# Optimization experiments

Hardware: AMD Instinct MI355X
Metric: run time of the kernel (lower is better)

## Reference

```python
import jax, jax.numpy as jnp
import numpy as np

B, H, N, T, E, D = 8, 8, 64, 256, 512, 64  # batch, heads, series, window, embed, feature
TAU = 1.0
DH = E // H  # per-head dim = 64


def setup_inputs() -> dict:
    key = jax.random.key(0)
    ks = jax.random.split(key, 7)
    f32 = jnp.float32
    return {
        "q": jax.random.normal(ks[0], (B, N, E), f32),
        "k": jax.random.normal(ks[1], (B, N, E), f32),
        "v": jax.random.normal(ks[2], (B, H, N, T, D), f32),
        # nn.Linear weights use torch (out, in) convention, bias=False
        "Wq": jax.random.normal(ks[3], (E, E), f32) * (E ** -0.5),
        "Wk": jax.random.normal(ks[4], (E, E), f32) * (E ** -0.5),
        # causal-convolution temporal mixing kernel per head/series
        "Wconv": jax.random.normal(ks[5], (H, N, T, T), f32) * (T ** -0.5),
        # concat projection: (out=D, in=H*D)
        "Wcat": jax.random.normal(ks[6], (D, H * D), f32) * ((H * D) ** -0.5),
    }


def reference(q, k, v, Wq, Wk, Wconv, Wcat):
    # Q/K projections, split into heads: (B,N,E) -> (B,H,N,DH)
    Q = (q @ Wq.T).reshape(B, N, H, DH).transpose(0, 2, 1, 3)
    K = (k @ Wk.T).reshape(B, N, H, DH).transpose(0, 2, 1, 3)

    # Causal convolution V projection: lower-triangular masked temporal mixing
    causal = jnp.tril(jnp.ones((T, T), v.dtype))
    V = jnp.einsum('hnts,bhnsd->bhntd', Wconv * causal, v)  # (B,H,N,T,D)

    # tau-scaled multi-head attention over the series axis
    scores = jnp.einsum('bhid,bhjd->bhij', Q, K) / (TAU * np.sqrt(DH).astype(np.float32))
    attn = jax.nn.softmax(scores, axis=-1)  # (B,H,N,N); dropout=0 (eval)
    out = jnp.einsum('bhij,bhjtd->bhitd', attn, V)  # (B,H,N,T,D)

    # reshape/permute chain == (B,H,N,T,D) -> (B,N,T,H*D)
    out = out.transpose(0, 2, 3, 1, 4).reshape(B, N, T, H * D)
    return out @ Wcat.T  # (B,N,T,D)
```

## Files before the change

kernel.cpp:

```cpp
#include <hip/hip_runtime.h>
#include <hip/hip_bf16.h>


typedef unsigned short u16;
typedef unsigned int u32;
typedef __attribute__((ext_vector_type(8))) short short8;
typedef __attribute__((ext_vector_type(4))) float f32x4;

static __device__ __forceinline__ u16 f2bf(float f) {
    u32 x; __builtin_memcpy(&x, &f, 4);
    u32 r = (x + 0x7fffu + ((x >> 16) & 1u)) >> 16;
    return (u16)r;
}
static __device__ __forceinline__ short8 pack8(float4 a, float4 b) {
    short8 r;
    r[0] = (short)f2bf(a.x); r[1] = (short)f2bf(a.y);
    r[2] = (short)f2bf(a.z); r[3] = (short)f2bf(a.w);
    r[4] = (short)f2bf(b.x); r[5] = (short)f2bf(b.y);
    r[6] = (short)f2bf(b.z); r[7] = (short)f2bf(b.w);
    return r;
}
static __device__ __forceinline__ short8 mk_bfrag(f32x4 a, f32x4 b) {
    u32 w0 = (__float_as_uint(a[0]) >> 16) | (__float_as_uint(a[1]) & 0xffff0000u);
    u32 w1 = (__float_as_uint(a[2]) >> 16) | (__float_as_uint(a[3]) & 0xffff0000u);
    u32 w2 = (__float_as_uint(b[0]) >> 16) | (__float_as_uint(b[1]) & 0xffff0000u);
    u32 w3 = (__float_as_uint(b[2]) >> 16) | (__float_as_uint(b[3]) & 0xffff0000u);
    uint4 u = make_uint4(w0, w1, w2, w3);
    short8 r; __builtin_memcpy(&r, &u, 16); return r;
}
static __device__ __forceinline__ short8 mk_bfrag_rnd(f32x4 a, f32x4 b) {
    short8 r;
    r[0] = (short)f2bf(a[0]); r[1] = (short)f2bf(a[1]);
    r[2] = (short)f2bf(a[2]); r[3] = (short)f2bf(a[3]);
    r[4] = (short)f2bf(b[0]); r[5] = (short)f2bf(b[1]);
    r[6] = (short)f2bf(b[2]); r[7] = (short)f2bf(b[3]);
    return r;
}
static __device__ __forceinline__ uint2 pk4(f32x4 d) {
    return make_uint2((__float_as_uint(d[0]) >> 16) | (__float_as_uint(d[1]) & 0xffff0000u),
                      (__float_as_uint(d[2]) >> 16) | (__float_as_uint(d[3]) & 0xffff0000u));
}

__global__ __launch_bounds__(256) void proj_qk(
        const float* __restrict__ q, const float* __restrict__ k,
        const float* __restrict__ Wq, const float* __restrict__ Wk,
        float* __restrict__ Qh, float* __restrict__ Kh) {
    const int et = blockIdx.x, rt = blockIdx.y, z = blockIdx.z;
    const float* X = z ? k : q;
    const float* W = z ? Wk : Wq;
    float* Out = z ? Kh : Qh;
    __shared__ float Xs[32][65];
    __shared__ float Ws[32][65];
    const int tid = threadIdx.x;
    const int tx = tid & 15, ty = tid >> 4;
    const int r0 = rt * 64, e0 = et * 64;
    float acc[4][4] = {};
    for (int k0 = 0; k0 < 512; k0 += 32) {
        __syncthreads();
        #pragma unroll
        for (int rep = 0; rep < 8; ++rep) {
            int lin = rep * 256 + tid;
            int kk = lin & 31, m = lin >> 5;
            Xs[kk][m] = X[(size_t)(r0 + m) * 512 + k0 + kk];
            Ws[kk][m] = W[(size_t)(e0 + m) * 512 + k0 + kk];
        }
        __syncthreads();
        #pragma unroll 8
        for (int kk = 0; kk < 32; ++kk) {
            float a0 = Xs[kk][4 * ty + 0], a1 = Xs[kk][4 * ty + 1];
            float a2 = Xs[kk][4 * ty + 2], a3 = Xs[kk][4 * ty + 3];
            float b0 = Ws[kk][4 * tx + 0], b1 = Ws[kk][4 * tx + 1];
            float b2 = Ws[kk][4 * tx + 2], b3 = Ws[kk][4 * tx + 3];
            acc[0][0] += a0 * b0; acc[0][1] += a0 * b1; acc[0][2] += a0 * b2; acc[0][3] += a0 * b3;
            acc[1][0] += a1 * b0; acc[1][1] += a1 * b1; acc[1][2] += a1 * b2; acc[1][3] += a1 * b3;
            acc[2][0] += a2 * b0; acc[2][1] += a2 * b1; acc[2][2] += a2 * b2; acc[2][3] += a2 * b3;
            acc[3][0] += a3 * b0; acc[3][1] += a3 * b1; acc[3][2] += a3 * b2; acc[3][3] += a3 * b3;
        }
    }
    #pragma unroll
    for (int i = 0; i < 4; ++i) {
        #pragma unroll
        for (int j = 0; j < 4; ++j) {
            int r = r0 + 4 * ty + i;
            int e = e0 + 4 * tx + j;
            int b = r >> 6, n = r & 63, h = e >> 6, dh = e & 63;
            Out[(((size_t)(b * 8 + h) * 64 + n) * 64) + dh] = acc[i][j];
        }
    }
}

__global__ __launch_bounds__(256) void attn_softmax(
        const float* __restrict__ Qh, const float* __restrict__ Kh,
        u16* __restrict__ Aperm) {
    const int bh = blockIdx.x;
    const int b = bh >> 3, h = bh & 7;
    const int tid = threadIdx.x;
    __shared__ float Qt[64][64];
    __shared__ float KT[64][65];
    const size_t base = (size_t)bh * 4096;
    #pragma unroll
    for (int rep = 0; rep < 16; ++rep) {
        int lin = rep * 256 + tid;
        int r = lin >> 6, c = lin & 63;
        Qt[r][c] = Qh[base + lin];
        KT[c][r] = Kh[base + lin];
    }
    __syncthreads();
    const int w = tid >> 6, lane = tid & 63;
    const int w31 = lane & 31;
    const int slot = (w31 < 16) ? ((w31 >> 2) * 8 + (w31 & 3))
                                : (((w31 - 16) >> 2) * 8 + 4 + (w31 & 3));
    const int p = h * 64 + (lane & 32) + slot;
    for (int rr = 0; rr < 16; ++rr) {
        int i = w + 4 * rr;
        float s = 0.f;
        #pragma unroll
        for (int dd = 0; dd < 64; ++dd) s += Qt[i][dd] * KT[dd][lane];
        s *= 0.125f;
        float m = s;
        #pragma unroll
        for (int off = 32; off; off >>= 1) m = fmaxf(m, __shfl_xor(m, off));
        float e = __expf(s - m);
        float sum = e;
        #pragma unroll
        for (int off = 32; off; off >>= 1) sum += __shfl_xor(sum, off);
        Aperm[((size_t)(b * 64 + i) << 9) + p] = f2bf(e / sum);
    }
}

template<int TI, int OFF>
__device__ __forceinline__ void load_tile(short8 wc[18], const float* __restrict__ wcb,
                                          int lo, int hi) {
    const int t = TI * 16 + lo;
    #pragma unroll
    for (int kk = 0; kk <= TI / 2; ++kk) {
        const float* p = wcb + (size_t)t * 256 + kk * 32 + hi * 8;
        float4 x = ((const float4*)p)[0], y = ((const float4*)p)[1];
        float wf[8] = {x.x, x.y, x.z, x.w, y.x, y.y, y.z, y.w};
        if (kk == TI / 2) {
            int sb = kk * 32 + hi * 8;
            #pragma unroll
            for (int e = 0; e < 8; ++e)
                if (sb + e > t) wf[e] = 0.f;
        }
        short8 af;
        #pragma unroll
        for (int e = 0; e < 8; ++e) af[e] = (short)f2bf(wf[e]);
        wc[OFF + kk] = af;
    }
}

template<int W>
__device__ __forceinline__ void load_wconv_w(short8 wc[18], const float* __restrict__ wcb,
                                             int lo, int hi) {
    load_tile<2 * W,      0        >(wc, wcb, lo, hi);
    load_tile<2 * W + 1,  W + 1    >(wc, wcb, lo, hi);
    load_tile<14 - 2 * W, 2 * W + 2>(wc, wcb, lo, hi);
    load_tile<15 - 2 * W, 10 + W   >(wc, wcb, lo, hi);
}

template<int M, int OA, int OB, int TB>
__device__ __forceinline__ void pair_conv_store(const short8 wc[18],
        const u16* __restrict__ vptB, u16* __restrict__ vout,
        int lo, int hi, short8 J1, short8 J2) {
    f32x4 aA[4] = {}, aB[4] = {};
    #pragma unroll
    for (int kk = 0; kk <= M; ++kk) {
        short8 bfr[4];
        #pragma unroll
        for (int di = 0; di < 4; ++di) {
            int d = di * 16 + lo;
            int sc = kk * 4 + hi;
            bfr[di] = *(const short8*)&vptB[d * 256 + ((sc ^ (d & 7)) << 3)];
        }
        #pragma unroll
        for (int di = 0; di < 4; ++di) {
            aA[di] = __builtin_amdgcn_mfma_f32_16x16x32_bf16(wc[OA + kk], bfr[di], aA[di], 0, 0, 0);
            aB[di] = __builtin_amdgcn_mfma_f32_16x16x32_bf16(wc[OB + kk], bfr[di], aB[di], 0, 0, 0);
        }
    }
    const f32x4 z = {};
    #pragma unroll
    for (int di = 0; di < 4; ++di) {
        short8 Xc = mk_bfrag_rnd(aA[di], aB[di]);
        f32x4 D1 = __builtin_amdgcn_mfma_f32_16x16x32_bf16(Xc, J1, z, 0, 0, 0);
        f32x4 D2 = __builtin_amdgcn_mfma_f32_16x16x32_bf16(Xc, J2, z, 0, 0, 0);
        *(uint2*)&vout[(size_t)(TB + lo) * 64 + di * 16 + hi * 4] = pk4(D1);
        *(uint2*)&vout[(size_t)(TB + 16 + lo) * 64 + di * 16 + hi * 4] = pk4(D2);
    }
}

template<int W>
__device__ __forceinline__ void phaseB_w(const short8 wc[18], const u16* __restrict__ vptB,
        u16* __restrict__ vout, int lo, int hi, short8 J1, short8 J2) {
    pair_conv_store<W,     0,         W + 1,  32 * W       >(wc, vptB, vout, lo, hi, J1, J2);
    pair_conv_store<7 - W, 2 * W + 2, 10 + W, (14 - 2 * W) * 16>(wc, vptB, vout, lo, hi, J1, J2);
}

__global__ __launch_bounds__(256, 2) void conv_mfma(
        const float* __restrict__ v, const float* __restrict__ Wconv,
        const float* __restrict__ Wcat, u16* __restrict__ Vp,
        int b0, int bs, int nsplit) {
    const int bid = blockIdx.x;
    const int split = (nsplit > 1) ? ((bid >> 3) & 1) : 0;
    const int hj = (nsplit > 1) ? (((bid >> 4) << 3) | (bid & 7)) : bid;
    const int h = hj >> 6, j = hj & 63;
    const int tid = threadIdx.x;
    const int w = tid >> 6, l = tid & 63;
    const int lo = l & 15, hi = l >> 4;
    const int bstart = b0 + split * bs;
    const int blbase = split * bs;

    __shared__ u16 vptB[2][64 * 256];

    short8 J1, J2;
    #pragma unroll
    for (int e = 0; e < 8; ++e) {
        int pie = (e < 4) ? (hi * 4 + e) : (16 + hi * 4 + (e - 4));
        J1[e] = (pie == lo) ? (short)0x3F80 : (short)0;
        J2[e] = (pie == lo + 16) ? (short)0x3F80 : (short)0;
    }

    short8 wc[18];
    const float* wcb = Wconv + (size_t)hj * 65536;
    if (w == 0)      load_wconv_w<0>(wc, wcb, lo, hi);
    else if (w == 1) load_wconv_w<1>(wc, wcb, lo, hi);
    else if (w == 2) load_wconv_w<2>(wc, wcb, lo, hi);
    else             load_wconv_w<3>(wc, wcb, lo, hi);

    short8 wcat[2][4];
    #pragma unroll
    for (int kk = 0; kk < 2; ++kk)
        #pragma unroll
        for (int di = 0; di < 4; ++di) {
            const float* p = Wcat + (size_t)(di * 16 + lo) * 512 + h * 64 + kk * 32 + hi * 8;
            wcat[kk][di] = pack8(((const float4*)p)[0], ((const float4*)p)[1]);
        }

    for (int i = 0; i < bs; ++i) {
        const int b = bstart + i;
        u16* buf = vptB[i & 1];
        const size_t vb = ((size_t)(b * 8 + h) * 64 + j) * 16384;
        #pragma unroll
        for (int si = 0; si < 4; ++si) {
            const float* p = v + vb + (size_t)(w * 64 + si * 16 + lo) * 64;
            f32x4 a4[4] = {};
            #pragma unroll
            for (int kk = 0; kk < 2; ++kk) {
                const float4* q = (const float4*)(p + kk * 32 + hi * 8);
                short8 af = pack8(q[0], q[1]);
                #pragma unroll
                for (int di = 0; di < 4; ++di)
                    a4[di] = __builtin_amdgcn_mfma_f32_16x16x32_bf16(af, wcat[kk][di], a4[di], 0, 0, 0);
            }
            int s0 = w * 64 + si * 16 + hi * 4;
            #pragma unroll
            for (int di = 0; di < 4; ++di) {
                int d = di * 16 + lo;
                u32 lo32 = (u32)f2bf(a4[di][0]) | ((u32)f2bf(a4[di][1]) << 16);
                u32 hi32 = (u32)f2bf(a4[di][2]) | ((u32)f2bf(a4[di][3]) << 16);
                *(uint2*)&buf[d * 256 + (((s0 >> 3) ^ (d & 7)) << 3) + (s0 & 7)] =
                    make_uint2(lo32, hi32);
            }
        }
        __syncthreads();
        u16* vout = Vp + ((size_t)(blbase + i) * 512 + hj) * 16384;
        if (w == 0)      phaseB_w<0>(wc, buf, vout, lo, hi, J1, J2);
        else if (w == 1) phaseB_w<1>(wc, buf, vout, lo, hi, J1, J2);
        else if (w == 2) phaseB_w<2>(wc, buf, vout, lo, hi, J1, J2);
        else             phaseB_w<3>(wc, buf, vout, lo, hi, J1, J2);
    }
}

__global__ __launch_bounds__(256) void final_mfma(
        const u16* __restrict__ Aperm, const u16* __restrict__ Vp,
        float* __restrict__ out, int bbase) {
    const int nblk = blockIdx.x;
    const int bl = blockIdx.y, b = bbase + bl;
    const int tid = threadIdx.x;
    const int w = tid >> 6, l = tid & 63;
    const int lo = l & 15, hi = l >> 4;
    const int nb = nblk * 128 + w * 32;

    short8 I1, I2;
    #pragma unroll
    for (int e = 0; e < 8; ++e) {
        I1[e] = (hi * 8 + e == lo) ? (short)0x3F80 : (short)0;
        I2[e] = (hi * 8 + e == lo + 16) ? (short)0x3F80 : (short)0;
    }

    const u16* ab = Aperm + ((size_t)b << 15);
    const u16* vb = Vp + (size_t)bl * 512 * 16384;

    f32x4 acc[4][2] = {};
    const f32x4 z = {};

    #define LDAF(af, k0) { \
        _Pragma("unroll") \
        for (int mi = 0; mi < 4; ++mi) \
            af[mi] = *(const short8*)&ab[(size_t)(mi * 16 + lo) * 512 + (k0) + hi * 8]; }
    #define LDX(X1, X2, k0) { \
        X1 = *(const short8*)&vb[(size_t)((k0) + lo) * 16384 + nb + hi * 8]; \
        X2 = *(const short8*)&vb[(size_t)((k0) + 16 + lo) * 16384 + nb + hi * 8]; }
    #define COMPUTE(af, X1, X2) { \
        f32x4 t1a = __builtin_amdgcn_mfma_f32_16x16x32_bf16(X1, I1, z, 0, 0, 0); \
        f32x4 t1b = __builtin_amdgcn_mfma_f32_16x16x32_bf16(X1, I2, z, 0, 0, 0); \
        f32x4 t2a = __builtin_amdgcn_mfma_f32_16x16x32_bf16(X2, I1, z, 0, 0, 0); \
        f32x4 t2b = __builtin_amdgcn_mfma_f32_16x16x32_bf16(X2, I2, z, 0, 0, 0); \
        short8 B0 = mk_bfrag(t1a, t2a); \
        short8 B1 = mk_bfrag(t1b, t2b); \
        _Pragma("unroll") \
        for (int mi = 0; mi < 4; ++mi) { \
            acc[mi][0] = __builtin_amdgcn_mfma_f32_16x16x32_bf16(af[mi], B0, acc[mi][0], 0, 0, 0); \
            acc[mi][1] = __builtin_amdgcn_mfma_f32_16x16x32_bf16(af[mi], B1, acc[mi][1], 0, 0, 0); \
        } }

    short8 afA[4], afB[4], X1A, X2A, X1B, X2B;
    LDAF(afA, 0); LDX(X1A, X2A, 0);
    #pragma unroll
    for (int ks = 0; ks < 16; ks += 2) {
        const int k1 = (ks + 1) * 32;
        const int k2 = ((ks + 2) & 15) * 32;
        LDAF(afB, k1); LDX(X1B, X2B, k1);
        COMPUTE(afA, X1A, X2A);
        LDAF(afA, k2); LDX(X1A, X2A, k2);
        COMPUTE(afB, X1B, X2B);
    }
    #undef LDAF
    #undef LDX
    #undef COMPUTE

    float* ob = out + ((size_t)b << 20);
    #pragma unroll
    for (int mi = 0; mi < 4; ++mi) {
        #pragma unroll
        for (int nt = 0; nt < 2; ++nt) {
            int td = nb + nt * 16 + lo;
            #pragma unroll
            for (int r = 0; r < 4; ++r) {
                int i = mi * 16 + hi * 4 + r;
                ob[(size_t)i * 16384 + td] = acc[mi][nt][r];
            }
        }
    }
}

extern "C" void kernel_launch(void* const* d_in, const int* in_sizes, int n_in,
                              void* d_out, int out_size, void* d_ws, size_t ws_size,
                              hipStream_t stream) {
    const float* q     = (const float*)d_in[0];
    const float* k     = (const float*)d_in[1];
    const float* v     = (const float*)d_in[2];
    const float* Wq    = (const float*)d_in[3];
    const float* Wk    = (const float*)d_in[4];
    const float* Wconv = (const float*)d_in[5];
    const float* Wcat  = (const float*)d_in[6];
    float* out = (float*)d_out;

    u16* Aperm = (u16*)d_ws;
    float* Qh = (float*)(Aperm + 262144);
    float* Kh = Qh + 262144;
    u16* Vp = (u16*)(Kh + 262144);
    const size_t fixed = 262144 * 2 + (size_t)2 * 262144 * 4;

    int bc = 8;
    while (bc > 1 && fixed + (size_t)bc * 512 * 16384 * 2 > ws_size) bc >>= 1;

    proj_qk<<<dim3(8, 8, 2), 256, 0, stream>>>(q, k, Wq, Wk, Qh, Kh);
    attn_softmax<<<64, 256, 0, stream>>>(Qh, Kh, Aperm);
    for (int b0 = 0; b0 < 8; b0 += bc) {
        int nsplit = (bc + 3) / 4;
        int bs = bc / nsplit;
        conv_mfma<<<dim3(nsplit * 512), 256, 0, stream>>>(v, Wconv, Wcat, Vp, b0, bs, nsplit);
        final_mfma<<<dim3(128, bc), 256, 0, stream>>>(Aperm, Vp, out, b0);
    }
}
```

Baseline: 226.2 us.

## Split conv work across eight waves per block and stage Wcat in LDS

The causal-conv kernel now runs 512 threads (8 waves) per (head,series) block instead of 4 waves, with each wave owning one paired time tile (W and 15-W), so Wconv registers per wave drop from 18 to 9 fragments. The batch split across two blocks is removed, so each block loops over all batches in its chunk with a single LDS buffer guarded by extra barriers. Wcat is packed once into swizzled LDS and reread per batch instead of being held in registers. The aim is more waves resident per CU and lower register pressure, at the cost of fewer blocks (512) and an added barrier per iteration that drops the double-buffer overlap.

Measured after the change: 219.6 us, median of 2. 1.03x faster.

```diff
diff --git a/kernel.cpp b/kernel.cpp
--- a/kernel.cpp
+++ b/kernel.cpp
@@ -129,7 +129,7 @@
 }
 
 template<int TI, int OFF>
-__device__ __forceinline__ void load_tile(short8 wc[18], const float* __restrict__ wcb,
+__device__ __forceinline__ void load_tile(short8* wc, const float* __restrict__ wcb,
                                           int lo, int hi) {
     const int t = TI * 16 + lo;
     #pragma unroll
@@ -151,21 +151,19 @@
 }
 
 template<int W>
-__device__ __forceinline__ void load_wconv_w(short8 wc[18], const float* __restrict__ wcb,
+__device__ __forceinline__ void load_wconv_w(short8 wc[9], const float* __restrict__ wcb,
                                              int lo, int hi) {
-    load_tile<2 * W,      0        >(wc, wcb, lo, hi);
-    load_tile<2 * W + 1,  W + 1    >(wc, wcb, lo, hi);
-    load_tile<14 - 2 * W, 2 * W + 2>(wc, wcb, lo, hi);
-    load_tile<15 - 2 * W, 10 + W   >(wc, wcb, lo, hi);
-}
-
-template<int M, int OA, int OB, int TB>
-__device__ __forceinline__ void pair_conv_store(const short8 wc[18],
-        const u16* __restrict__ vptB, u16* __restrict__ vout,
-        int lo, int hi, short8 J1, short8 J2) {
+    load_tile<W,      0        >(wc, wcb, lo, hi);
+    load_tile<15 - W, W / 2 + 1>(wc, wcb, lo, hi);
+}
+
+template<int W>
+__device__ __forceinline__ void phaseB_w(const short8 wc[9], const u16* __restrict__ vptB,
+        u16* __restrict__ vout, int lo, int hi, short8 J1) {
+    constexpr int KA = W / 2, KB = (15 - W) / 2, OB = KA + 1;
     f32x4 aA[4] = {}, aB[4] = {};
     #pragma unroll
-    for (int kk = 0; kk <= M; ++kk) {
+    for (int kk = 0; kk <= KB; ++kk) {
         short8 bfr[4];
         #pragma unroll
         for (int di = 0; di < 4; ++di) {
@@ -175,100 +173,111 @@
         }
         #pragma unroll
         for (int di = 0; di < 4; ++di) {
-            aA[di] = __builtin_amdgcn_mfma_f32_16x16x32_bf16(wc[OA + kk], bfr[di], aA[di], 0, 0, 0);
             aB[di] = __builtin_amdgcn_mfma_f32_16x16x32_bf16(wc[OB + kk], bfr[di], aB[di], 0, 0, 0);
+            if (kk <= KA)
+                aA[di] = __builtin_amdgcn_mfma_f32_16x16x32_bf16(wc[kk], bfr[di], aA[di], 0, 0, 0);
         }
     }
     const f32x4 z = {};
     #pragma unroll
     for (int di = 0; di < 4; ++di) {
-        short8 Xc = mk_bfrag_rnd(aA[di], aB[di]);
-        f32x4 D1 = __builtin_amdgcn_mfma_f32_16x16x32_bf16(Xc, J1, z, 0, 0, 0);
-        f32x4 D2 = __builtin_amdgcn_mfma_f32_16x16x32_bf16(Xc, J2, z, 0, 0, 0);
-        *(uint2*)&vout[(size_t)(TB + lo) * 64 + di * 16 + hi * 4] = pk4(D1);
-        *(uint2*)&vout[(size_t)(TB + 16 + lo) * 64 + di * 16 + hi * 4] = pk4(D2);
-    }
-}
-
-template<int W>
-__device__ __forceinline__ void phaseB_w(const short8 wc[18], const u16* __restrict__ vptB,
-        u16* __restrict__ vout, int lo, int hi, short8 J1, short8 J2) {
-    pair_conv_store<W,     0,         W + 1,  32 * W       >(wc, vptB, vout, lo, hi, J1, J2);
-    pair_conv_store<7 - W, 2 * W + 2, 10 + W, (14 - 2 * W) * 16>(wc, vptB, vout, lo, hi, J1, J2);
-}
-
-__global__ __launch_bounds__(256, 2) void conv_mfma(
+        short8 XcA = mk_bfrag_rnd(aA[di], aA[di]);
+        short8 XcB = mk_bfrag_rnd(aB[di], aB[di]);
+        f32x4 DA = __builtin_amdgcn_mfma_f32_16x16x32_bf16(XcA, J1, z, 0, 0, 0);
+        f32x4 DB = __builtin_amdgcn_mfma_f32_16x16x32_bf16(XcB, J1, z, 0, 0, 0);
+        *(uint2*)&vout[(size_t)(W * 16 + lo) * 64 + di * 16 + hi * 4] = pk4(DA);
+        *(uint2*)&vout[(size_t)((15 - W) * 16 + lo) * 64 + di * 16 + hi * 4] = pk4(DB);
+    }
+}
+
+__global__ __launch_bounds__(512, 4) void conv_mfma(
         const float* __restrict__ v, const float* __restrict__ Wconv,
         const float* __restrict__ Wcat, u16* __restrict__ Vp,
-        int b0, int bs, int nsplit) {
-    const int bid = blockIdx.x;
-    const int split = (nsplit > 1) ? ((bid >> 3) & 1) : 0;
-    const int hj = (nsplit > 1) ? (((bid >> 4) << 3) | (bid & 7)) : bid;
-    const int h = hj >> 6, j = hj & 63;
+        int b0, int bs) {
+    const int hj = blockIdx.x, h = hj >> 6, j = hj & 63;
     const int tid = threadIdx.x;
     const int w = tid >> 6, l = tid & 63;
     const int lo = l & 15, hi = l >> 4;
-    const int bstart = b0 + split * bs;
-    const int blbase = split * bs;
-
-    __shared__ u16 vptB[2][64 * 256];
-
-    short8 J1, J2;
+
+    __shared__ u16 vptB[64 * 256];
+    __shared__ u16 wcatL[64 * 64];
+
+    short8 J1;
     #pragma unroll
     for (int e = 0; e < 8; ++e) {
         int pie = (e < 4) ? (hi * 4 + e) : (16 + hi * 4 + (e - 4));
         J1[e] = (pie == lo) ? (short)0x3F80 : (short)0;
-        J2[e] = (pie == lo + 16) ? (short)0x3F80 : (short)0;
-    }
-
-    short8 wc[18];
+    }
+
+    short8 wc[9];
     const float* wcb = Wconv + (size_t)hj * 65536;
     if (w == 0)      load_wconv_w<0>(wc, wcb, lo, hi);
     else if (w == 1) load_wconv_w<1>(wc, wcb, lo, hi);
     else if (w == 2) load_wconv_w<2>(wc, wcb, lo, hi);
-    else             load_wconv_w<3>(wc, wcb, lo, hi);
-
-    short8 wcat[2][4];
-    #pragma unroll
-    for (int kk = 0; kk < 2; ++kk)
-        #pragma unroll
-        for (int di = 0; di < 4; ++di) {
-            const float* p = Wcat + (size_t)(di * 16 + lo) * 512 + h * 64 + kk * 32 + hi * 8;
-            wcat[kk][di] = pack8(((const float4*)p)[0], ((const float4*)p)[1]);
-        }
+    else if (w == 3) load_wconv_w<3>(wc, wcb, lo, hi);
+    else if (w == 4) load_wconv_w<4>(wc, wcb, lo, hi);
+    else if (w == 5) load_wconv_w<5>(wc, wcb, lo, hi);
+    else if (w == 6) load_wconv_w<6>(wc, wcb, lo, hi);
+    else             load_wconv_w<7>(wc, wcb, lo, hi);
+
+    {
+        int lin = tid * 8;
+        int d = lin >> 6, dd0 = lin & 63;
+        const float* p = Wcat + (size_t)d * 512 + h * 64 + dd0;
+        short8 wv = pack8(((const float4*)p)[0], ((const float4*)p)[1]);
+        *(short8*)&wcatL[d * 64 + (((dd0 >> 3) ^ (d & 7)) << 3)] = wv;
+    }
+    asm volatile("s_waitcnt lgkmcnt(0)" ::: "memory");
+    __builtin_amdgcn_s_barrier();
 
     for (int i = 0; i < bs; ++i) {
-        const int b = bstart + i;
-        u16* buf = vptB[i & 1];
+        const int b = b0 + i;
+        short8 wcat[2][4];
+        #pragma unroll
+        for (int kk = 0; kk < 2; ++kk)
+            #pragma unroll
+            for (int di = 0; di < 4; ++di) {
+                int d = di * 16 + lo;
+                int c8 = kk * 4 + hi;
+                wcat[kk][di] = *(const short8*)&wcatL[d * 64 + ((c8 ^ (d & 7)) << 3)];
+            }
         const size_t vb = ((size_t)(b * 8 + h) * 64 + j) * 16384;
         #pragma unroll
-        for (int si = 0; si < 4; ++si) {
-            const float* p = v + vb + (size_t)(w * 64 + si * 16 + lo) * 64;
+        for (int si = 0; si < 2; ++si) {
+            const float* p = v + vb + (size_t)(w * 32 + si * 16 + lo) * 64;
+            const float4* q0 = (const float4*)(p + hi * 8);
+            const float4* q1 = (const float4*)(p + 32 + hi * 8);
+            short8 af0 = pack8(q0[0], q0[1]);
+            short8 af1 = pack8(q1[0], q1[1]);
             f32x4 a4[4] = {};
             #pragma unroll
-            for (int kk = 0; kk < 2; ++kk) {
-                const float4* q = (const float4*)(p + kk * 32 + hi * 8);
-                short8 af = pack8(q[0], q[1]);
-                #pragma unroll
-                for (int di = 0; di < 4; ++di)
-                    a4[di] = __builtin_amdgcn_mfma_f32_16x16x32_bf16(af, wcat[kk][di], a4[di], 0, 0, 0);
+            for (int di = 0; di < 4; ++di) {
+                a4[di] = __builtin_amdgcn_mfma_f32_16x16x32_bf16(af0, wcat[0][di], a4[di], 0, 0, 0);
+                a4[di] = __builtin_amdgcn_mfma_f32_16x16x32_bf16(af1, wcat[1][di], a4[di], 0, 0, 0);
             }
-            int s0 = w * 64 + si * 16 + hi * 4;
+            int s0 = w * 32 + si * 16 + hi * 4;
             #pragma unroll
             for (int di = 0; di < 4; ++di) {
                 int d = di * 16 + lo;
                 u32 lo32 = (u32)f2bf(a4[di][0]) | ((u32)f2bf(a4[di][1]) << 16);
                 u32 hi32 = (u32)f2bf(a4[di][2]) | ((u32)f2bf(a4[di][3]) << 16);
-                *(uint2*)&buf[d * 256 + (((s0 >> 3) ^ (d & 7)) << 3) + (s0 & 7)] =
+                *(uint2*)&vptB[d * 256 + (((s0 >> 3) ^ (d & 7)) << 3) + (s0 & 7)] =
                     make_uint2(lo32, hi32);
             }
         }
-        __syncthreads();
-        u16* vout = Vp + ((size_t)(blbase + i) * 512 + hj) * 16384;
-        if (w == 0)      phaseB_w<0>(wc, buf, vout, lo, hi, J1, J2);
-        else if (w == 1) phaseB_w<1>(wc, buf, vout, lo, hi, J1, J2);
-        else if (w == 2) phaseB_w<2>(wc, buf, vout, lo, hi, J1, J2);
-        else             phaseB_w<3>(wc, buf, vout, lo, hi, J1, J2);
+        asm volatile("s_waitcnt lgkmcnt(0)" ::: "memory");
+        __builtin_amdgcn_s_barrier();
+        u16* vout = Vp + ((size_t)i * 512 + hj) * 16384;
+        if (w == 0)      phaseB_w<0>(wc, vptB, vout, lo, hi, J1);
+        else if (w == 1) phaseB_w<1>(wc, vptB, vout, lo, hi, J1);
+        else if (w == 2) phaseB_w<2>(wc, vptB, vout, lo, hi, J1);
+        else if (w == 3) phaseB_w<3>(wc, vptB, vout, lo, hi, J1);
+        else if (w == 4) phaseB_w<4>(wc, vptB, vout, lo, hi, J1);
+        else if (w == 5) phaseB_w<5>(wc, vptB, vout, lo, hi, J1);
+        else if (w == 6) phaseB_w<6>(wc, vptB, vout, lo, hi, J1);
+        else             phaseB_w<7>(wc, vptB, vout, lo, hi, J1);
+        asm volatile("s_waitcnt lgkmcnt(0)" ::: "memory");
+        __builtin_amdgcn_s_barrier();
     }
 }
 
@@ -369,9 +378,7 @@
     proj_qk<<<dim3(8, 8, 2), 256, 0, stream>>>(q, k, Wq, Wk, Qh, Kh);
     attn_softmax<<<64, 256, 0, stream>>>(Qh, Kh, Aperm);
     for (int b0 = 0; b0 < 8; b0 += bc) {
-        int nsplit = (bc + 3) / 4;
-        int bs = bc / nsplit;
-        conv_mfma<<<dim3(nsplit * 512), 256, 0, stream>>>(v, Wconv, Wcat, Vp, b0, bs, nsplit);
+        conv_mfma<<<dim3(512), 512, 0, stream>>>(v, Wconv, Wcat, Vp, b0, bc);
         final_mfma<<<dim3(128, bc), 256, 0, stream>>>(Aperm, Vp, out, b0);
     }
 }
```
